# Performance work log

Hardware: AMD Instinct MI355X
Metric: run time of the kernel (lower is better)

Reference implementation:

```python
import jax, jax.numpy as jnp
import numpy as np

N_HEAD, D_HEAD, D_MODEL = 8, 64, 512
MEM_LEN, QLEN, BSZ = 1024, 1024, 4
KLEN = MEM_LEN + QLEN
CONV_PAD = 3  # conv_size // 2 for conv_size = 7
LN_EPS = 1e-5


def setup_inputs() -> dict:
    key = jax.random.key(0)
    ks = jax.random.split(key, 16)
    s = 0.02
    inp = {
        "w": jax.random.normal(ks[0], (QLEN, BSZ, D_MODEL), jnp.float32),
        "r": jax.random.normal(ks[1], (KLEN, D_MODEL), jnp.float32),
        "mems": jax.random.normal(ks[2], (MEM_LEN, BSZ, D_MODEL), jnp.float32),
        "r_w_bias": jax.random.normal(ks[3], (N_HEAD, D_HEAD), jnp.float32) * s,
        "r_r_bias": jax.random.normal(ks[4], (N_HEAD, D_HEAD), jnp.float32) * s,
        "qkv_W": jax.random.normal(ks[5], (3 * N_HEAD * D_HEAD, D_MODEL), jnp.float32) * s,
        "r_W": jax.random.normal(ks[6], (N_HEAD * D_HEAD, D_MODEL), jnp.float32) * s,
        "conv_q_w": jax.random.normal(ks[7], (D_HEAD, D_HEAD, 7), jnp.float32) * 0.05,
        "conv_q_b": jnp.zeros((D_HEAD,), jnp.float32),
        "conv_k_w": jax.random.normal(ks[8], (D_HEAD, D_HEAD, 7), jnp.float32) * 0.05,
        "conv_k_b": jnp.zeros((D_HEAD,), jnp.float32),
        "conv_v_w": jax.random.normal(ks[9], (D_HEAD, D_HEAD, 7), jnp.float32) * 0.05,
        "conv_v_b": jnp.zeros((D_HEAD,), jnp.float32),
        "o_W": jax.random.normal(ks[10], (D_MODEL, N_HEAD * D_HEAD), jnp.float32) * s,
        "ln_g": jnp.ones((D_MODEL,), jnp.float32),
        "ln_b": jnp.zeros((D_MODEL,), jnp.float32),
        # causal-with-memory mask: query i may attend keys j <= i + MEM_LEN
        "attn_mask": jnp.arange(KLEN)[None, :] > (jnp.arange(QLEN)[:, None] + MEM_LEN),
    }
    return inp


def _conv1d(x, wt, b):
    # x: [N, C, L], wt: [O, I, K], same padding (pad=3)
    y = jax.lax.conv_general_dilated(x, wt, (1,), [(CONV_PAD, CONV_PAD)],
                                     dimension_numbers=("NCH", "OIH", "NCH"))
    return y + b[None, :, None]


def _head_conv(x, wt, b, length, bsz):
    # x: [len, b, H*Dh] -> per-head Conv1d over time -> [len, b, H, Dh]
    xh = x.reshape(length, bsz, N_HEAD, D_HEAD).transpose(2, 1, 3, 0)  # [H,b,Dh,len]
    xh = xh.reshape(N_HEAD * bsz, D_HEAD, length)
    xh = _conv1d(xh, wt, b)
    return xh.reshape(N_HEAD, bsz, D_HEAD, length).transpose(3, 1, 0, 2)  # [len,b,H,Dh]


def _rel_shift(x):
    # x: [qlen, rlen, b, n]
    q, rl, b, n = x.shape
    zp = jnp.zeros((q, 1, b, n), x.dtype)
    xp = jnp.concatenate([zp, x], axis=1).reshape(rl + 1, q, b, n)[1:]
    return xp.reshape(q, rl, b, n)


def _layer_norm(x, g, b):
    mu = jnp.mean(x, axis=-1, keepdims=True)
    var = jnp.mean(jnp.square(x - mu), axis=-1, keepdims=True)
    return (x - mu) * jax.lax.rsqrt(var + LN_EPS) * g + b


def reference(w, r, mems, r_w_bias, r_r_bias, qkv_W, r_W,
              conv_q_w, conv_q_b, conv_k_w, conv_k_b, conv_v_w, conv_v_b,
              o_W, ln_g, ln_b, attn_mask):
    qlen, bsz = w.shape[0], w.shape[1]
    cat = jnp.concatenate([mems, w], axis=0)           # [klen, b, d_model]
    klen = cat.shape[0]
    w_heads = cat @ qkv_W.T                            # [klen, b, 3*H*Dh]
    r_head_k = (r @ r_W.T).reshape(klen, N_HEAD, D_HEAD)
    q, k, v = jnp.split(w_heads, 3, axis=-1)
    q = q[-qlen:]
    # per-head conv augmentation of Q/K/V
    q = _head_conv(q, conv_q_w, conv_q_b, qlen, bsz)   # [qlen,b,H,Dh]
    k = _head_conv(k, conv_k_w, conv_k_b, klen, bsz)   # [klen,b,H,Dh]
    v = _head_conv(v, conv_v_w, conv_v_b, klen, bsz)
    scale = 1.0 / (D_HEAD ** 0.5)
    AC = jnp.einsum("ibnd,jbnd->ijbn", q + r_w_bias, k)
    BD = jnp.einsum("ibnd,jnd->ijbn", q + r_r_bias, r_head_k)
    BD = _rel_shift(BD)
    attn_score = (AC + BD) * scale                     # [qlen,klen,b,H]
    attn_score = jnp.where(attn_mask[:, :, None, None], -jnp.inf, attn_score)
    attn_prob = jax.nn.softmax(attn_score, axis=1)
    attn_vec = jnp.einsum("ijbn,jbnd->ibnd", attn_prob, v)
    attn_vec = attn_vec.reshape(qlen, bsz, N_HEAD * D_HEAD)
    attn_out = attn_vec @ o_W.T                        # [qlen,b,d_model]
    return _layer_norm(w + attn_out, ln_g, ln_b)
```

## Files before the change

kernel.cpp:

```cpp
#include <hip/hip_runtime.h>
#include <hip/hip_bf16.h>

typedef unsigned short u16;
typedef unsigned int   u32;
typedef u16 u16x8 __attribute__((ext_vector_type(8)));
typedef u16 u16x4 __attribute__((ext_vector_type(4)));
typedef float f32x4 __attribute__((ext_vector_type(4)));
typedef short s16x8 __attribute__((ext_vector_type(8)));
typedef u32 u32x4 __attribute__((ext_vector_type(4)));

__device__ __forceinline__ float b2f(u16 u) { return __uint_as_float(((u32)u) << 16); }
__device__ __forceinline__ u16 f2b(float f) {
  u32 u = __float_as_uint(f);
  u32 r = u + 0x7FFFu + ((u >> 16) & 1u);
  return (u16)(r >> 16);
}
__device__ __forceinline__ u32 f2b2(float lo, float hi) {
  __hip_bfloat162 h = __float22bfloat162_rn(make_float2(lo, hi));
  union { __hip_bfloat162 h; u32 u; } cv;
  cv.h = h;
  return cv.u;
}

#define MFMA_B16(A, B, C) __builtin_amdgcn_mfma_f32_16x16x32_bf16((A), (B), (C), 0, 0, 0)

__device__ __forceinline__ void gl16(const u16* g, u16* l) {
  __builtin_amdgcn_global_load_lds(
      (const __attribute__((address_space(1))) void*)g,
      (__attribute__((address_space(3))) void*)l, 16, 0, 0);
}

__global__ __launch_bounds__(256) void cvt_all(
    const float* __restrict__ mems, const float* __restrict__ w,
    const float* __restrict__ r, const float* __restrict__ qkvW,
    const float* __restrict__ rW, const float* __restrict__ oW,
    const float* __restrict__ cqw, const float* __restrict__ ckw,
    const float* __restrict__ cvw,
    u16* __restrict__ catb, u16* __restrict__ rb, u16* __restrict__ qkvWb,
    u16* __restrict__ rWb, u16* __restrict__ oWb, u16* __restrict__ cwb) {
  if (blockIdx.x >= 3200) {
    int idx = (blockIdx.x - 3200) * 256 + threadIdx.x;
    if (idx >= 86016) return;
    int wsel = idx / 28672, rem = idx % 28672;
    const float* src = (wsel == 0) ? cqw : ((wsel == 1) ? ckw : cvw);
    int s = rem / 4096, r2 = rem % 4096;
    int d = r2 / 64, eswz = r2 % 64;
    int e = (((eswz >> 3) ^ (d & 7)) << 3) + (eswz & 7);
    cwb[idx] = f2b(src[d * 448 + e * 7 + s]);
    return;
  }
  long g = ((long)blockIdx.x * 256 + threadIdx.x) * 8;
  const float* src;
  u16* dst;
  if (g < 4194304) {
    src = (g < 2097152) ? (mems + g) : (w + (g - 2097152));
    dst = catb + g;
  } else if (g < 5242880) {
    src = r + (g - 4194304);    dst = rb + (g - 4194304);
  } else if (g < 6029312) {
    src = qkvW + (g - 5242880); dst = qkvWb + (g - 5242880);
  } else if (g < 6291456) {
    src = rW + (g - 6029312);   dst = rWb + (g - 6029312);
  } else {
    src = oW + (g - 6291456);   dst = oWb + (g - 6291456);
  }
  f32x4 a = *(const f32x4*)src;
  f32x4 b = *(const f32x4*)(src + 4);
  u32x4 p = (u32x4){f2b2(a[0], a[1]), f2b2(a[2], a[3]),
                    f2b2(b[0], b[1]), f2b2(b[2], b[3])};
  *(u32x4*)dst = p;
}

__global__ __launch_bounds__(256) void gemm_fused(
    const u16* __restrict__ catb, const u16* __restrict__ qkvWb,
    u16* __restrict__ Wh, const u16* __restrict__ rb,
    const u16* __restrict__ rWb, u16* __restrict__ Rk) {
  int bx = blockIdx.x, by = blockIdx.y;
  const u16 *A, *B;
  u16* C;
  int N;
  if (bx < 12) {
    if (bx < 4 && by < 32) return;
    A = catb; B = qkvWb; C = Wh; N = 1536;
  } else {
    if (by >= 16) return;
    A = rb; B = rWb; C = Rk; N = 512; bx = 0;
  }
  const int K = 512;
  __shared__ u16 A_s[128 * 32];
  __shared__ u16 B_s[128 * 32];
  int tid = threadIdx.x;
  int wave = tid >> 6, lane = tid & 63, quad = lane >> 4, l16 = lane & 15;
  int wr = wave >> 1, wc = wave & 1;

  f32x4 acc[4][4];
#pragma unroll
  for (int a = 0; a < 4; a++)
#pragma unroll
    for (int bb = 0; bb < 4; bb++) acc[a][bb] = (f32x4){0.f, 0.f, 0.f, 0.f};

  const u16* Ab = A + (size_t)by * 128 * K;
  const u16* Bb = B + (size_t)bx * 128 * K;
  int lrow = lane >> 2;
  int lkc  = (lane & 3) * 8;
  int L0 = wave * 2;

  for (int k0 = 0; k0 < K; k0 += 32) {
    __syncthreads();
#pragma unroll
    for (int m = 0; m < 2; m++) {
      int L = L0 + m;
      int row = L * 16 + lrow;
      gl16(Ab + (size_t)row * K + k0 + lkc, &A_s[L * 512 + lane * 8]);
      gl16(Bb + (size_t)row * K + k0 + lkc, &B_s[L * 512 + lane * 8]);
    }
    __syncthreads();

    s16x8 af[4], bf[4];
#pragma unroll
    for (int a = 0; a < 4; a++)
      af[a] = *(const s16x8*)&A_s[(wr * 64 + a * 16 + l16) * 32 + quad * 8];
#pragma unroll
    for (int bb = 0; bb < 4; bb++)
      bf[bb] = *(const s16x8*)&B_s[(wc * 64 + bb * 16 + l16) * 32 + quad * 8];
#pragma unroll
    for (int a = 0; a < 4; a++)
#pragma unroll
      for (int bb = 0; bb < 4; bb++)
        acc[a][bb] = MFMA_B16(af[a], bf[bb], acc[a][bb]);
  }

#pragma unroll
  for (int a = 0; a < 4; a++)
#pragma unroll
    for (int bb = 0; bb < 4; bb++) {
      int row = by * 128 + wr * 64 + a * 16 + quad * 4;
      int col = bx * 128 + wc * 64 + bb * 16 + l16;
#pragma unroll
      for (int reg = 0; reg < 4; reg++)
        C[(size_t)(row + reg) * N + col] = f2b(acc[a][bb][reg]);
    }
}

__global__ __launch_bounds__(256) void gemm_mfma(
    const u16* __restrict__ A, const u16* __restrict__ B,
    u16* __restrict__ C, int N, int K) {
  __shared__ u16 A_s[64 * 32];
  __shared__ u16 B_s[128 * 32];
  int tid = threadIdx.x;
  int bx = blockIdx.x, by = blockIdx.y;
  int wave = tid >> 6, lane = tid & 63, quad = lane >> 4, l16 = lane & 15;
  int lrow = lane >> 2;
  int lkc  = (lane & 3) * 8;
  int L0 = wave * 2;

  f32x4 acc[4][2];
#pragma unroll
  for (int a = 0; a < 4; a++)
#pragma unroll
    for (int bb = 0; bb < 2; bb++) acc[a][bb] = (f32x4){0.f, 0.f, 0.f, 0.f};

  const u16* Ab = A + (size_t)by * 64 * K;
  const u16* Bb = B + (size_t)bx * 128 * K;

  for (int k0 = 0; k0 < K; k0 += 32) {
    __syncthreads();
    gl16(Ab + (size_t)(wave * 16 + lrow) * K + k0 + lkc, &A_s[wave * 512 + lane * 8]);
#pragma unroll
    for (int m = 0; m < 2; m++) {
      int L = L0 + m;
      int row = L * 16 + lrow;
      gl16(Bb + (size_t)row * K + k0 + lkc, &B_s[L * 512 + lane * 8]);
    }
    __syncthreads();

    s16x8 af[4], bf[2];
#pragma unroll
    for (int a = 0; a < 4; a++)
      af[a] = *(const s16x8*)&A_s[(a * 16 + l16) * 32 + quad * 8];
#pragma unroll
    for (int bb = 0; bb < 2; bb++)
      bf[bb] = *(const s16x8*)&B_s[(wave * 32 + bb * 16 + l16) * 32 + quad * 8];
#pragma unroll
    for (int a = 0; a < 4; a++)
#pragma unroll
      for (int bb = 0; bb < 2; bb++)
        acc[a][bb] = MFMA_B16(af[a], bf[bb], acc[a][bb]);
  }

#pragma unroll
  for (int a = 0; a < 4; a++)
#pragma unroll
    for (int bb = 0; bb < 2; bb++) {
      int row = by * 64 + a * 16 + quad * 4;
      int col = bx * 128 + wave * 32 + bb * 16 + l16;
#pragma unroll
      for (int reg = 0; reg < 4; reg++)
        C[(size_t)(row + reg) * N + col] = f2b(acc[a][bb][reg]);
    }
}

__global__ __launch_bounds__(256) void conv_fused(
    const u16* __restrict__ Wh, const u16* __restrict__ cwb,
    const float* __restrict__ cqb, const float* __restrict__ ckb,
    const float* __restrict__ cvb,
    u16* __restrict__ qpost, u16* __restrict__ kpost, u16* __restrict__ vpostT) {
  __shared__ u16 wT_s[7 * 4096];
  __shared__ u16 in_s[134 * 64];
  int blk = blockIdx.x;
  int part, lt0, len, tshift, vt;
  const float* cbp;
  const u16* cwp;
  u16* outp;
  if (blk < 2) {
    part = 0; lt0 = blk * 4; len = 1024; tshift = 1024; vt = 0;
    cbp = cqb; cwp = cwb; outp = qpost;
  } else if (blk < 6) {
    part = 1; lt0 = (blk - 2) * 4; len = 2048; tshift = 0; vt = 0;
    cbp = ckb; cwp = cwb + 28672; outp = kpost;
  } else {
    part = 2; lt0 = (blk - 6) * 4; len = 2048; tshift = 0; vt = 1;
    cbp = cvb; cwp = cwb + 57344; outp = vpostT;
  }
  int tid = threadIdx.x;
  int b = blockIdx.y, n = blockIdx.z;
  int wave = tid >> 6, lane = tid & 63, quad = lane >> 4, l16 = lane & 15;

  for (int idx = tid * 8; idx < 28672; idx += 2048)
    *(u16x8*)&wT_s[idx] = *(const u16x8*)(cwp + idx);

  float bias[4];
#pragma unroll
  for (int nn = 0; nn < 4; nn++) bias[nn] = cbp[nn * 16 + l16];

  int e8 = tid & 7;
  int colb = part * 512 + n * 64 + e8 * 8;

  for (int ch = 0; ch < 4; ch++) {
    int t0 = (lt0 + ch) * 128;
    if (ch) __syncthreads();
    for (int r = tid >> 3; r < 134; r += 32) {
      int tt = t0 + r - 3;
      u16x8 v = {0, 0, 0, 0, 0, 0, 0, 0};
      if (tt >= 0 && tt < len)
        v = *(const u16x8*)(Wh + (size_t)((tt + tshift) * 4 + b) * 1536 + colb);
      *(u16x8*)&in_s[r * 64 + ((e8 ^ (r & 7)) << 3)] = v;
    }
    __syncthreads();

    f32x4 acc[2][4];
#pragma unroll
    for (int mt = 0; mt < 2; mt++)
#pragma unroll
      for (int nn = 0; nn < 4; nn++) acc[mt][nn] = (f32x4){0.f, 0.f, 0.f, 0.f};

#pragma unroll
    for (int s = 0; s < 7; s++) {
#pragma unroll
      for (int ks = 0; ks < 2; ks++) {
        int eb = ks * 4 + quad;
        s16x8 af[2];
#pragma unroll
        for (int mt = 0; mt < 2; mt++) {
          int r = wave * 32 + mt * 16 + l16 + s;
          af[mt] = *(const s16x8*)&in_s[r * 64 + ((eb ^ (r & 7)) << 3)];
        }
#pragma unroll
        for (int nn = 0; nn < 4; nn++) {
          int d = nn * 16 + l16;
          s16x8 bf = *(const s16x8*)&wT_s[s * 4096 + d * 64 + ((eb ^ (d & 7)) << 3)];
          acc[0][nn] = MFMA_B16(af[0], bf, acc[0][nn]);
          acc[1][nn] = MFMA_B16(af[1], bf, acc[1][nn]);
        }
      }
    }

    if (!vt) {
#pragma unroll
      for (int mt = 0; mt < 2; mt++)
#pragma unroll
        for (int nn = 0; nn < 4; nn++) {
          int col = nn * 16 + l16;
#pragma unroll
          for (int reg = 0; reg < 4; reg++) {
            int t = t0 + wave * 32 + mt * 16 + quad * 4 + reg;
            outp[(size_t)((t * 4 + b) * 8 + n) * 64 + col] = f2b(acc[mt][nn][reg] + bias[nn]);
          }
        }
    } else {
      __syncthreads();
      u16* T = in_s;
#pragma unroll
      for (int mt = 0; mt < 2; mt++)
#pragma unroll
        for (int nn = 0; nn < 4; nn++) {
          union { u32 u[2]; u16x4 v; } pk;
          pk.u[0] = f2b2(acc[mt][nn][0] + bias[nn], acc[mt][nn][1] + bias[nn]);
          pk.u[1] = f2b2(acc[mt][nn][2] + bias[nn], acc[mt][nn][3] + bias[nn]);
          *(u16x4*)&T[(nn * 16 + l16) * 132 + wave * 32 + mt * 16 + quad * 4] = pk.v;
        }
      __syncthreads();
      int dS = tid >> 2, tq = tid & 3;
      u16* gdst = outp + ((size_t)(b * 8 + n) * 64 + dS) * 2048 + t0 + tq * 32;
      const u16* tsrc = &T[dS * 132 + tq * 32];
#pragma unroll
      for (int c = 0; c < 4; c++)
        *(u16x8*)(gdst + c * 8) = *(const u16x8*)(tsrc + c * 8);
    }
  }
}

__global__ __launch_bounds__(256) void attn_mfma(
    const u16* __restrict__ qpost, const u16* __restrict__ kpost,
    const u16* __restrict__ vpostT, const u16* __restrict__ Rk,
    const float* __restrict__ rwb, const float* __restrict__ rrb,
    u16* __restrict__ av_out) {
  __shared__ u16 K_s[64 * 64];
  __shared__ u16 V_s[64 * 64];
  __shared__ u16 R_s[128 * 64];
  __shared__ u16 BD_s[4][80 * 20];
  __shared__ u16 P_s[4][16 * 64];
  int tid = threadIdx.x;
  int xc = blockIdx.x;
  int y  = blockIdx.y;
  int it = (y < 8) ? y : 23 - y;
  int i0 = it * 64;
  int b = xc >> 3, n = xc & 7;
  int wave = tid >> 6, lane = tid & 63, quad = lane >> 4, l16 = lane & 15;
  int i0w = i0 + wave * 16;
  int rbaseW = 48 - wave * 16;
  int rbase = 960 - i0;
  int ntiles = it + 17;
  const float SC = 0.125f * 1.44269504f;

  s16x8 aw[2], ar[2];
  {
    int ig = i0w + l16;
    const u16* qp = qpost + ((size_t)((ig * 4 + b) * 8 + n)) * 64;
#pragma unroll
    for (int ks = 0; ks < 2; ks++) {
      int d0 = ks * 32 + quad * 8;
      u16x8 qv = *(const u16x8*)(qp + d0);
      union { u32x4 u; s16x8 s; } pw, pr;
#pragma unroll
      for (int e2 = 0; e2 < 4; e2++) {
        float qa = b2f(qv[2 * e2]), qb = b2f(qv[2 * e2 + 1]);
        pw.u[e2] = f2b2(qa + rwb[n * 64 + d0 + 2 * e2], qb + rwb[n * 64 + d0 + 2 * e2 + 1]);
        pr.u[e2] = f2b2(qa + rrb[n * 64 + d0 + 2 * e2], qb + rrb[n * 64 + d0 + 2 * e2 + 1]);
      }
      aw[ks] = pw.s;
      ar[ks] = pr.s;
    }
  }

  {
    int rrI = tid >> 1, h = tid & 1;
    int g = rbase + rrI;
    int prow = g & 127;
    const u16* rp2 = Rk + (size_t)g * 512 + n * 64 + h * 32;
#pragma unroll
    for (int c = 0; c < 4; c++) {
      int kb = h * 4 + c;
      *(u16x8*)&R_s[prow * 64 + ((kb ^ (prow & 7)) << 3)] = *(const u16x8*)(rp2 + c * 8);
    }
  }

  f32x4 O[4];
#pragma unroll
  for (int c = 0; c < 4; c++) O[c] = (f32x4){0.f, 0.f, 0.f, 0.f};
  float l4[4] = {0.f, 0.f, 0.f, 0.f};

  int jl = tid >> 2, q4 = tid & 3;
  u16x8 kv0, kv1, vv0, vv1, rv0, rv1;
  {
    size_t src = ((size_t)(jl * 4 + b) * 8 + n) * 64 + q4 * 16;
    kv0 = *(const u16x8*)(kpost + src);
    kv1 = *(const u16x8*)(kpost + src + 8);
    const u16* vsrc = vpostT + ((size_t)(b * 8 + n) * 64 + jl) * 2048 + q4 * 16;
    vv0 = *(const u16x8*)(vsrc);
    vv1 = *(const u16x8*)(vsrc + 8);
  }
  {
    int g = rbase + 128 + jl;
    rv0 = (u16x8){0, 0, 0, 0, 0, 0, 0, 0};
    rv1 = rv0;
    if (g < 2048) {
      const u16* rp2 = Rk + (size_t)g * 512 + n * 64 + q4 * 16;
      rv0 = *(const u16x8*)(rp2);
      rv1 = *(const u16x8*)(rp2 + 8);
    }
  }

  for (int t = 0; t < ntiles; t++) {
    int j0 = t * 64;
    __syncthreads();
    *(u16x8*)&K_s[jl * 64 + (((2 * q4) ^ (jl & 7)) << 3)] = kv0;
    *(u16x8*)&K_s[jl * 64 + (((2 * q4 + 1) ^ (jl & 7)) << 3)] = kv1;
    *(u16x8*)&V_s[jl * 64 + (((2 * q4) ^ (jl & 7)) << 3)] = vv0;
    *(u16x8*)&V_s[jl * 64 + (((2 * q4 + 1) ^ (jl & 7)) << 3)] = vv1;
    if (t > 0) {
      int g = rbase + j0 + 64 + jl;
      int prow = g & 127;
      *(u16x8*)&R_s[prow * 64 + (((2 * q4) ^ (prow & 7)) << 3)] = rv0;
      *(u16x8*)&R_s[prow * 64 + (((2 * q4 + 1) ^ (prow & 7)) << 3)] = rv1;
    }
    __syncthreads();

    if (t + 1 < ntiles) {
      int j0n = j0 + 64;
      size_t src = ((size_t)((j0n + jl) * 4 + b) * 8 + n) * 64 + q4 * 16;
      kv0 = *(const u16x8*)(kpost + src);
      kv1 = *(const u16x8*)(kpost + src + 8);
      const u16* vsrc = vpostT + ((size_t)(b * 8 + n) * 64 + jl) * 2048 + j0n + q4 * 16;
      vv0 = *(const u16x8*)(vsrc);
      vv1 = *(const u16x8*)(vsrc + 8);
      int g = rbase + j0n + 64 + jl;
      rv0 = (u16x8){0, 0, 0, 0, 0, 0, 0, 0};
      rv1 = rv0;
      if (g < 2048) {
        const u16* rp2 = Rk + (size_t)g * 512 + n * 64 + q4 * 16;
        rv0 = *(const u16x8*)(rp2);
        rv1 = *(const u16x8*)(rp2 + 8);
      }
    }

    f32x4 sc4[4];
#pragma unroll
    for (int c = 0; c < 4; c++) {
      f32x4 tt = (f32x4){0.f, 0.f, 0.f, 0.f};
#pragma unroll
      for (int ks = 0; ks < 2; ks++) {
        int j = c * 16 + l16;
        int kb = ks * 4 + quad;
        s16x8 kf = *(const s16x8*)&K_s[j * 64 + ((kb ^ (j & 7)) << 3)];
        tt = MFMA_B16(aw[ks], kf, tt);
      }
      sc4[c] = tt;
    }
    int rbj = rbase + j0 + rbaseW;
#pragma unroll
    for (int cb = 0; cb < 5; cb++) {
      f32x4 tt = (f32x4){0.f, 0.f, 0.f, 0.f};
#pragma unroll
      for (int ks = 0; ks < 2; ks++) {
        int prow = (rbj + cb * 16 + l16) & 127;
        int kb = ks * 4 + quad;
        s16x8 rf = *(const s16x8*)&R_s[prow * 64 + ((kb ^ (prow & 7)) << 3)];
        tt = MFMA_B16(ar[ks], rf, tt);
      }
      union { u32 u[2]; u16x4 v; } pk;
      pk.u[0] = f2b2(tt[0], tt[1]);
      pk.u[1] = f2b2(tt[2], tt[3]);
      *(u16x4*)&BD_s[wave][(cb * 16 + l16) * 20 + quad * 4] = pk.v;
    }

#pragma unroll
    for (int c = 0; c < 4; c++)
#pragma unroll
      for (int reg = 0; reg < 4; reg++) {
        int iw = quad * 4 + reg;
        int uw = c * 16 + l16 + 15 - iw;
        float bd = b2f(BD_s[wave][uw * 20 + iw]);
        float val = (sc4[c][reg] + bd) * SC;
        int jg = j0 + c * 16 + l16;
        float p = (jg > i0w + iw + 1024) ? 0.f : __builtin_amdgcn_exp2f(val);
        l4[reg] += p;
        int jb = c * 2 + (l16 >> 3);
        P_s[wave][iw * 64 + ((jb ^ (iw & 7)) << 3) + (l16 & 7)] = f2b(p);
      }

#pragma unroll
    for (int cd = 0; cd < 4; cd++) {
      int d = cd * 16 + l16;
#pragma unroll
      for (int ks = 0; ks < 2; ks++) {
        int kb = ks * 4 + quad;
        s16x8 pf = *(const s16x8*)&P_s[wave][l16 * 64 + ((kb ^ (l16 & 7)) << 3)];
        s16x8 vf = *(const s16x8*)&V_s[d * 64 + ((kb ^ (d & 7)) << 3)];
        O[cd] = MFMA_B16(pf, vf, O[cd]);
      }
    }
  }

#pragma unroll
  for (int off = 1; off < 16; off <<= 1)
#pragma unroll
    for (int reg = 0; reg < 4; reg++) l4[reg] += __shfl_xor(l4[reg], off);

#pragma unroll
  for (int reg = 0; reg < 4; reg++) {
    float inv = 1.0f / l4[reg];
    int ig2 = i0w + quad * 4 + reg;
#pragma unroll
    for (int cd = 0; cd < 4; cd++)
      av_out[((size_t)(ig2 * 4 + b)) * 512 + n * 64 + cd * 16 + l16] =
          f2b(O[cd][reg] * inv);
  }
}

__global__ __launch_bounds__(64) void lnorm(
    const float* __restrict__ w, const u16* __restrict__ ao,
    const float* __restrict__ g, const float* __restrict__ bb,
    float* __restrict__ out) {
  int row = blockIdx.x, t = threadIdx.x;
  const float* wp = w + (size_t)row * 512 + t * 8;
  const u16* ap = ao + (size_t)row * 512 + t * 8;
  f32x4 w0 = *(const f32x4*)wp;
  f32x4 w1 = *(const f32x4*)(wp + 4);
  u16x8 av = *(const u16x8*)ap;
  float x[8];
  float sum = 0.f;
#pragma unroll
  for (int e = 0; e < 4; e++) {
    x[e] = w0[e] + b2f(av[e]);
    x[4 + e] = w1[e] + b2f(av[4 + e]);
  }
#pragma unroll
  for (int e = 0; e < 8; e++) sum += x[e];
#pragma unroll
  for (int off = 1; off < 64; off <<= 1) sum += __shfl_xor(sum, off);
  float mu = sum * (1.0f / 512.0f);
  float vs = 0.f;
#pragma unroll
  for (int e = 0; e < 8; e++) {
    float d = x[e] - mu;
    vs += d * d;
  }
#pragma unroll
  for (int off = 1; off < 64; off <<= 1) vs += __shfl_xor(vs, off);
  float rs = rsqrtf(vs * (1.0f / 512.0f) + 1e-5f);
  f32x4 g0 = *(const f32x4*)(g + t * 8);
  f32x4 g1 = *(const f32x4*)(g + t * 8 + 4);
  f32x4 b0 = *(const f32x4*)(bb + t * 8);
  f32x4 b1 = *(const f32x4*)(bb + t * 8 + 4);
  f32x4 o0, o1;
#pragma unroll
  for (int e = 0; e < 4; e++) {
    o0[e] = (x[e] - mu) * rs * g0[e] + b0[e];
    o1[e] = (x[4 + e] - mu) * rs * g1[e] + b1[e];
  }
  float* op = out + (size_t)row * 512 + t * 8;
  *(f32x4*)op = o0;
  *(f32x4*)(op + 4) = o1;
}

extern "C" void kernel_launch(void* const* d_in, const int* in_sizes, int n_in,
                              void* d_out, int out_size, void* d_ws, size_t ws_size,
                              hipStream_t stream) {
  (void)in_sizes; (void)n_in; (void)out_size;
  const float* w    = (const float*)d_in[0];
  const float* r    = (const float*)d_in[1];
  const float* mems = (const float*)d_in[2];
  const float* rwb  = (const float*)d_in[3];
  const float* rrb  = (const float*)d_in[4];
  const float* qkvW = (const float*)d_in[5];
  const float* rW   = (const float*)d_in[6];
  const float* cqw  = (const float*)d_in[7];
  const float* cqb  = (const float*)d_in[8];
  const float* ckw  = (const float*)d_in[9];
  const float* ckb  = (const float*)d_in[10];
  const float* cvw  = (const float*)d_in[11];
  const float* cvb  = (const float*)d_in[12];
  const float* oW   = (const float*)d_in[13];
  const float* lng  = (const float*)d_in[14];
  const float* lnb  = (const float*)d_in[15];

  u16* ws     = (u16*)d_ws;
  u16* Wh     = ws;
  u16* qpost  = Wh + 12582912;
  u16* kpost  = qpost + 2097152;
  u16* vpostT = kpost + 4194304;
  u16* Rk     = vpostT + 4194304;
  u16* av     = Rk + 1048576;
  u16* aout   = av + 2097152;
  u16* qkvWb  = aout + 2097152;
  u16* rWb    = qkvWb + 786432;
  u16* oWb    = rWb + 262144;
  u16* cwb    = oWb + 262144;
  u16* catb   = av;
  u16* rb     = qpost;
  if (ws_size < 59416576ull) return;

  cvt_all<<<3536, 256, 0, stream>>>(mems, w, r, qkvW, rW, oW, cqw, ckw, cvw,
                                    catb, rb, qkvWb, rWb, oWb, cwb);
  gemm_fused<<<dim3(13, 64), 256, 0, stream>>>(catb, qkvWb, Wh, rb, rWb, Rk);
  conv_fused<<<dim3(10, 4, 8), 256, 0, stream>>>(Wh, cwb, cqb, ckb, cvb, qpost, kpost, vpostT);
  attn_mfma<<<dim3(32, 16), 256, 0, stream>>>(qpost, kpost, vpostT, Rk, rwb, rrb, av);
  gemm_mfma<<<dim3(4, 64), 256, 0, stream>>>(av, oWb, aout, 512, 512);
  lnorm<<<4096, 64, 0, stream>>>(w, aout, lng, lnb, (float*)d_out);
}
```

Before: 227.8 us.

## Fuse output projection GEMM with residual add and layer norm

Replaces the separate o-projection GEMM and layernorm kernels with one kernel where each block computes 16 full output rows across all 512 columns, then adds the residual and normalizes in registers with a cross-wave reduction through shared memory. This removes the bf16 intermediate write/read and one launch. In exchange every block reloads the full oW matrix, parallelism drops to 256 blocks, and variance is computed in a single pass (E[x^2]-mu^2).

```diff
diff --git a/kernel.cpp b/kernel.cpp
--- a/kernel.cpp
+++ b/kernel.cpp
@@ -142,62 +142,98 @@
     }
 }
 
-__global__ __launch_bounds__(256) void gemm_mfma(
-    const u16* __restrict__ A, const u16* __restrict__ B,
-    u16* __restrict__ C, int N, int K) {
-  __shared__ u16 A_s[64 * 32];
-  __shared__ u16 B_s[128 * 32];
+__global__ __launch_bounds__(256) void oproj_ln(
+    const u16* __restrict__ av, const u16* __restrict__ oWb,
+    const float* __restrict__ w, const float* __restrict__ lng,
+    const float* __restrict__ lnb, float* __restrict__ out) {
+  __shared__ u16 A_s[16 * 32];
+  __shared__ u16 B_s[512 * 32];
+  __shared__ float red_s[2][16][4];
   int tid = threadIdx.x;
-  int bx = blockIdx.x, by = blockIdx.y;
+  int by = blockIdx.x;
   int wave = tid >> 6, lane = tid & 63, quad = lane >> 4, l16 = lane & 15;
-  int lrow = lane >> 2;
-  int lkc  = (lane & 3) * 8;
-  int L0 = wave * 2;
-
-  f32x4 acc[4][2];
-#pragma unroll
-  for (int a = 0; a < 4; a++)
-#pragma unroll
-    for (int bb = 0; bb < 2; bb++) acc[a][bb] = (f32x4){0.f, 0.f, 0.f, 0.f};
-
-  const u16* Ab = A + (size_t)by * 64 * K;
-  const u16* Bb = B + (size_t)bx * 128 * K;
-
-  for (int k0 = 0; k0 < K; k0 += 32) {
-    __syncthreads();
-    gl16(Ab + (size_t)(wave * 16 + lrow) * K + k0 + lkc, &A_s[wave * 512 + lane * 8]);
-#pragma unroll
-    for (int m = 0; m < 2; m++) {
-      int L = L0 + m;
-      int row = L * 16 + lrow;
-      gl16(Bb + (size_t)row * K + k0 + lkc, &B_s[L * 512 + lane * 8]);
-    }
-    __syncthreads();
-
-    s16x8 af[4], bf[2];
-#pragma unroll
-    for (int a = 0; a < 4; a++)
-      af[a] = *(const s16x8*)&A_s[(a * 16 + l16) * 32 + quad * 8];
-#pragma unroll
-    for (int bb = 0; bb < 2; bb++)
-      bf[bb] = *(const s16x8*)&B_s[(wave * 32 + bb * 16 + l16) * 32 + quad * 8];
-#pragma unroll
-    for (int a = 0; a < 4; a++)
-#pragma unroll
-      for (int bb = 0; bb < 2; bb++)
-        acc[a][bb] = MFMA_B16(af[a], bf[bb], acc[a][bb]);
-  }
-
-#pragma unroll
-  for (int a = 0; a < 4; a++)
-#pragma unroll
-    for (int bb = 0; bb < 2; bb++) {
-      int row = by * 64 + a * 16 + quad * 4;
-      int col = bx * 128 + wave * 32 + bb * 16 + l16;
-#pragma unroll
-      for (int reg = 0; reg < 4; reg++)
-        C[(size_t)(row + reg) * N + col] = f2b(acc[a][bb][reg]);
-    }
+
+  f32x4 acc[8];
+#pragma unroll
+  for (int f = 0; f < 8; f++) acc[f] = (f32x4){0.f, 0.f, 0.f, 0.f};
+
+  const u16* Ab = av + (size_t)by * 16 * 512;
+  for (int k0 = 0; k0 < 512; k0 += 32) {
+    __syncthreads();
+    if (wave == 0) {
+      gl16(Ab + (size_t)(lane >> 2) * 512 + k0 + (lane & 3) * 8, &A_s[lane * 8]);
+    }
+#pragma unroll
+    for (int rr = 0; rr < 8; rr++) {
+      int row = (tid >> 2) + rr * 64;
+      gl16(oWb + (size_t)row * 512 + k0 + (tid & 3) * 8,
+           &B_s[row * 32 + (tid & 3) * 8]);
+    }
+    __syncthreads();
+
+    s16x8 af = *(const s16x8*)&A_s[l16 * 32 + quad * 8];
+#pragma unroll
+    for (int f = 0; f < 8; f++) {
+      int col = wave * 128 + f * 16 + l16;
+      s16x8 bf = *(const s16x8*)&B_s[col * 32 + quad * 8];
+      acc[f] = MFMA_B16(af, bf, acc[f]);
+    }
+  }
+
+  int rowb = by * 16;
+  float xs[8][4];
+  float psum[4] = {0.f, 0.f, 0.f, 0.f};
+  float psq[4]  = {0.f, 0.f, 0.f, 0.f};
+#pragma unroll
+  for (int f = 0; f < 8; f++) {
+    int col = wave * 128 + f * 16 + l16;
+#pragma unroll
+    for (int reg = 0; reg < 4; reg++) {
+      int row = rowb + quad * 4 + reg;
+      float x = w[(size_t)row * 512 + col] + acc[f][reg];
+      xs[f][reg] = x;
+      psum[reg] += x;
+      psq[reg]  += x * x;
+    }
+  }
+#pragma unroll
+  for (int off = 1; off < 16; off <<= 1)
+#pragma unroll
+    for (int reg = 0; reg < 4; reg++) {
+      psum[reg] += __shfl_xor(psum[reg], off);
+      psq[reg]  += __shfl_xor(psq[reg], off);
+    }
+  if (l16 == 0) {
+#pragma unroll
+    for (int reg = 0; reg < 4; reg++) {
+      red_s[0][quad * 4 + reg][wave] = psum[reg];
+      red_s[1][quad * 4 + reg][wave] = psq[reg];
+    }
+  }
+  __syncthreads();
+
+  float mu[4], rs[4];
+#pragma unroll
+  for (int reg = 0; reg < 4; reg++) {
+    int rw = quad * 4 + reg;
+    float s  = red_s[0][rw][0] + red_s[0][rw][1] + red_s[0][rw][2] + red_s[0][rw][3];
+    float sq = red_s[1][rw][0] + red_s[1][rw][1] + red_s[1][rw][2] + red_s[1][rw][3];
+    float m = s * (1.0f / 512.0f);
+    float v = sq * (1.0f / 512.0f) - m * m;
+    mu[reg] = m;
+    rs[reg] = rsqrtf(v + 1e-5f);
+  }
+
+#pragma unroll
+  for (int f = 0; f < 8; f++) {
+    int col = wave * 128 + f * 16 + l16;
+    float gv = lng[col], bv = lnb[col];
+#pragma unroll
+    for (int reg = 0; reg < 4; reg++) {
+      int row = rowb + quad * 4 + reg;
+      out[(size_t)row * 512 + col] = (xs[f][reg] - mu[reg]) * rs[reg] * gv + bv;
+    }
+  }
 }
 
 __global__ __launch_bounds__(256) void conv_fused(
@@ -498,52 +534,6 @@
   }
 }
 
-__global__ __launch_bounds__(64) void lnorm(
-    const float* __restrict__ w, const u16* __restrict__ ao,
-    const float* __restrict__ g, const float* __restrict__ bb,
-    float* __restrict__ out) {
-  int row = blockIdx.x, t = threadIdx.x;
-  const float* wp = w + (size_t)row * 512 + t * 8;
-  const u16* ap = ao + (size_t)row * 512 + t * 8;
-  f32x4 w0 = *(const f32x4*)wp;
-  f32x4 w1 = *(const f32x4*)(wp + 4);
-  u16x8 av = *(const u16x8*)ap;
-  float x[8];
-  float sum = 0.f;
-#pragma unroll
-  for (int e = 0; e < 4; e++) {
-    x[e] = w0[e] + b2f(av[e]);
-    x[4 + e] = w1[e] + b2f(av[4 + e]);
-  }
-#pragma unroll
-  for (int e = 0; e < 8; e++) sum += x[e];
-#pragma unroll
-  for (int off = 1; off < 64; off <<= 1) sum += __shfl_xor(sum, off);
-  float mu = sum * (1.0f / 512.0f);
-  float vs = 0.f;
-#pragma unroll
-  for (int e = 0; e < 8; e++) {
-    float d = x[e] - mu;
-    vs += d * d;
-  }
-#pragma unroll
-  for (int off = 1; off < 64; off <<= 1) vs += __shfl_xor(vs, off);
-  float rs = rsqrtf(vs * (1.0f / 512.0f) + 1e-5f);
-  f32x4 g0 = *(const f32x4*)(g + t * 8);
-  f32x4 g1 = *(const f32x4*)(g + t * 8 + 4);
-  f32x4 b0 = *(const f32x4*)(bb + t * 8);
-  f32x4 b1 = *(const f32x4*)(bb + t * 8 + 4);
-  f32x4 o0, o1;
-#pragma unroll
-  for (int e = 0; e < 4; e++) {
-    o0[e] = (x[e] - mu) * rs * g0[e] + b0[e];
-    o1[e] = (x[4 + e] - mu) * rs * g1[e] + b1[e];
-  }
-  float* op = out + (size_t)row * 512 + t * 8;
-  *(f32x4*)op = o0;
-  *(f32x4*)(op + 4) = o1;
-}
-
 extern "C" void kernel_launch(void* const* d_in, const int* in_sizes, int n_in,
                               void* d_out, int out_size, void* d_ws, size_t ws_size,
                               hipStream_t stream) {
@@ -586,6 +576,5 @@
   gemm_fused<<<dim3(13, 64), 256, 0, stream>>>(catb, qkvWb, Wh, rb, rWb, Rk);
   conv_fused<<<dim3(10, 4, 8), 256, 0, stream>>>(Wh, cwb, cqb, ckb, cvb, qpost, kpost, vpostT);
   attn_mfma<<<dim3(32, 16), 256, 0, stream>>>(qpost, kpost, vpostT, Rk, rwb, rrb, av);
-  gemm_mfma<<<dim3(4, 64), 256, 0, stream>>>(av, oWb, aout, 512, 512);
-  lnorm<<<4096, 64, 0, stream>>>(w, aout, lng, lnb, (float*)d_out);
-}
+  oproj_ln<<<256, 256, 0, stream>>>(av, oWb, w, lng, lnb, (float*)d_out);
+}
```

Measured after the change: 230.1 us. Within noise of the previous version (+1.0%).
